# Performance work log

Hardware: AMD Instinct MI355X
Metric: run time of the kernel (lower is better)

The kernel has to match this reference:

```python
import jax, jax.numpy as jnp
import numpy as np

POOL = 7          # pooling_regions
NUM_ROIS = 4
FEAT = 2048
NUM_CLASSES = 21


def _adaptive_avg_pool(crop, out=POOL):
    # crop: [C, Hc, Wc] with concrete (Python int) spatial sizes.
    # torch adaptive_avg_pool2d bins: start=floor(i*S/out), end=ceil((i+1)*S/out)
    C, Hc, Wc = crop.shape
    cs = jnp.cumsum(jnp.cumsum(crop, axis=1), axis=2)
    cs = jnp.pad(cs, ((0, 0), (1, 0), (1, 0)))  # integral image [C, Hc+1, Wc+1]
    i = np.arange(out)
    hs = np.floor(i * Hc / out).astype(np.int32)
    he = np.ceil((i + 1) * Hc / out).astype(np.int32)
    ws = np.floor(i * Wc / out).astype(np.int32)
    we = np.ceil((i + 1) * Wc / out).astype(np.int32)
    S = (cs[:, he[:, None], we[None, :]] - cs[:, hs[:, None], we[None, :]]
         - cs[:, he[:, None], ws[None, :]] + cs[:, hs[:, None], ws[None, :]])
    area = ((he - hs)[:, None] * (we - ws)[None, :]).astype(crop.dtype)
    return S / area  # [C, out, out]


def setup_inputs() -> dict:
    key = jax.random.key(0)
    ks = jax.random.split(key, 8)
    H = W = 128
    base_x = jax.random.normal(ks[0], (1, FEAT, H, W), dtype=jnp.float32)
    # rows are (x, y, h, w); crop = base_x[:, :, x:x+w, y:y+h]; fixed in-bounds boxes
    rois = jnp.array([[0, 0, 96, 96], [10, 20, 64, 80], [30, 5, 50, 70], [64, 64, 64, 64]], dtype=jnp.int32)
    red = FEAT // 4  # 512
    flat = red * POOL * POOL  # 25088
    conv_w = jax.random.normal(ks[1], (red, FEAT), dtype=jnp.float32) * 0.02   # 1x1 conv kernel
    conv_b = jnp.zeros((red,), dtype=jnp.float32)
    d1_w = jax.random.normal(ks[2], (2 * FEAT, flat), dtype=jnp.float32) * 0.01
    d1_b = jnp.zeros((2 * FEAT,), dtype=jnp.float32)
    d2_w = jax.random.normal(ks[3], (FEAT, 2 * FEAT), dtype=jnp.float32) * 0.01
    d2_b = jnp.zeros((FEAT,), dtype=jnp.float32)
    d3_w = jax.random.normal(ks[4], (NUM_CLASSES, FEAT), dtype=jnp.float32) * 0.01
    d4_w = jax.random.normal(ks[5], (4 * (NUM_CLASSES - 1), FEAT), dtype=jnp.float32) * 0.01
    return {"base_x": base_x, "rois": rois, "conv_w": conv_w, "conv_b": conv_b,
            "d1_w": d1_w, "d1_b": d1_b, "d2_w": d2_w, "d2_b": d2_b,
            "d3_w": d3_w, "d4_w": d4_w}


def reference(base_x, rois, conv_w, conv_b, d1_w, d1_b, d2_w, d2_b, d3_w, d4_w):
    rois_np = np.asarray(rois)  # concrete ROI coordinates (data-dependent crop shapes)
    pooled = []
    for rid in range(rois_np.shape[0]):
        x, y, h, w = (int(v) for v in rois_np[rid])
        crop = base_x[0, :, x:x + w, y:y + h]           # [FEAT, w, h]
        pooled.append(_adaptive_avg_pool(crop))          # [FEAT, 7, 7]
    out_roi_pool = jnp.stack(pooled, axis=0)             # [4, FEAT, 7, 7]
    # 1x1 conv reduction FEAT -> FEAT//4
    red = jnp.einsum('rchw,oc->rohw', out_roi_pool, conv_w) + conv_b[None, :, None, None]
    flat = red.reshape(NUM_ROIS, -1)                     # [4, 512*7*7]
    h1 = jax.nn.relu(flat @ d1_w.T + d1_b)               # dropout = identity (eval)
    h2 = jax.nn.relu(h1 @ d2_w.T + d2_b)
    out_class = jax.nn.softmax(h2 @ d3_w.T, axis=1)      # [4, num_classes]
    out_regr = h2 @ d4_w.T                               # [4, 4*(num_classes-1)]
    return (out_class, out_regr)
```

## Files before the change

kernel.cpp:

```cpp
#include <hip/hip_runtime.h>
#include <math.h>

#define FEAT   2048
#define RED    512
#define NROI   4
#define FLATSZ 25088
#define H1SZ   4096
#define H2SZ   2048
#define NCLS   21
#define NREG   80

__device__ __forceinline__ float wave_reduce_sum(float v) {
#pragma unroll
    for (int off = 32; off >= 1; off >>= 1)
        v += __shfl_xor(v, off, 64);
    return v;
}

__global__ __launch_bounds__(64) void pool_kernel(const float* __restrict__ base_x,
                                                  const int* __restrict__ rois,
                                                  float* __restrict__ pooled) {
    int bx   = blockIdx.x;
    int hb   = bx % 7;
    int c    = (bx / 7) % FEAT;
    int r    = bx / (7 * FEAT);
    int lane = threadIdx.x;

    const int* roi = rois + r * 4;
    int x = roi[0], y = roi[1];
    int Wc = roi[2];
    int Hc = roi[3];

    int hs = (hb * Hc) / 7;
    int he = ((hb + 1) * Hc + 6) / 7;

    int j0 = lane, j1 = lane + 64;
    int b00 = -1, b01 = -1, b10 = -1, b11 = -1;
#pragma unroll
    for (int b = 0; b < 7; ++b) {
        int wsb = (b * Wc) / 7;
        int web = ((b + 1) * Wc + 6) / 7;
        if (j0 >= wsb && j0 < web) { if (b00 < 0) b00 = b; else b01 = b; }
        if (j1 >= wsb && j1 < web) { if (b10 < 0) b10 = b; else b11 = b; }
    }

    const float* plane = base_x + (size_t)c * 16384 + y;
    float s0 = 0.f, s1 = 0.f;
    for (int i = hs; i < he; ++i) {
        const float* rowp = plane + (size_t)(x + i) * 128;
        if (j0 < Wc) s0 += rowp[j0];
        if (j1 < Wc) s1 += rowp[j1];
    }

    float hspan = (float)(he - hs);
#pragma unroll
    for (int b = 0; b < 7; ++b) {
        float v = (((b == b00) || (b == b01)) ? s0 : 0.f) +
                  (((b == b10) || (b == b11)) ? s1 : 0.f);
        v = wave_reduce_sum(v);
        if (lane == 0) {
            int wsb = (b * Wc) / 7;
            int web = ((b + 1) * Wc + 6) / 7;
            float area = hspan * (float)(web - wsb);
            pooled[((size_t)r * FEAT + c) * 49 + hb * 7 + b] = v / area;
        }
    }
}

__global__ __launch_bounds__(256) void conv_kernel(const float* __restrict__ pooled,
                                                   const float* __restrict__ conv_w,
                                                   const float* __restrict__ conv_b,
                                                   float* __restrict__ flat) {
    int bx = blockIdx.x;
    int r  = bx >> 7;
    int o0 = (bx & 127) * 4;
    int tid  = threadIdx.x;
    int wave = tid >> 6, lane = tid & 63;
    int hw = lane < 49 ? lane : 48;

    const float* pp  = pooled + (size_t)r * FEAT * 49 + hw;
    const float* w0p = conv_w + (size_t)(o0 + 0) * FEAT;
    const float* w1p = conv_w + (size_t)(o0 + 1) * FEAT;
    const float* w2p = conv_w + (size_t)(o0 + 2) * FEAT;
    const float* w3p = conv_w + (size_t)(o0 + 3) * FEAT;

    float a0 = 0.f, a1 = 0.f, a2 = 0.f, a3 = 0.f;
    int c0 = wave * 512;
#pragma unroll 8
    for (int c = c0; c < c0 + 512; ++c) {
        float v = pp[(size_t)c * 49];
        a0 += w0p[c] * v;
        a1 += w1p[c] * v;
        a2 += w2p[c] * v;
        a3 += w3p[c] * v;
    }

    __shared__ float lds[4][4][64];
    lds[wave][0][lane] = a0;
    lds[wave][1][lane] = a1;
    lds[wave][2][lane] = a2;
    lds[wave][3][lane] = a3;
    __syncthreads();

    if (lane < 49) {
        int od = wave;
        float v = lds[0][od][lane] + lds[1][od][lane] + lds[2][od][lane] + lds[3][od][lane];
        flat[(size_t)r * FLATSZ + (size_t)(o0 + od) * 49 + lane] = v + conv_b[o0 + od];
    }
}

#define DOT4(a, b) ((a).x * (b).x + (a).y * (b).y + (a).z * (b).z + (a).w * (b).w)

template <int K4, int ACT_LD, int OUT_LD, bool RELU>
__global__ __launch_bounds__(256) void gemv_rows4(const float* __restrict__ act,
                                                  const float* __restrict__ w,
                                                  const float* __restrict__ bias,
                                                  float* __restrict__ out) {
    const int j0  = blockIdx.x * 4;
    const int tid = threadIdx.x;
    const int K   = K4 * 4;

    const float4* w0 = (const float4*)(w + (size_t)(j0 + 0) * K);
    const float4* w1 = (const float4*)(w + (size_t)(j0 + 1) * K);
    const float4* w2 = (const float4*)(w + (size_t)(j0 + 2) * K);
    const float4* w3 = (const float4*)(w + (size_t)(j0 + 3) * K);
    const float4* a0 = (const float4*)(act + 0 * (size_t)ACT_LD);
    const float4* a1 = (const float4*)(act + 1 * (size_t)ACT_LD);
    const float4* a2 = (const float4*)(act + 2 * (size_t)ACT_LD);
    const float4* a3 = (const float4*)(act + 3 * (size_t)ACT_LD);

    float acc[16];
#pragma unroll
    for (int i = 0; i < 16; ++i) acc[i] = 0.f;

    for (int k = tid; k < K4; k += 256) {
        float4 va0 = a0[k], va1 = a1[k], va2 = a2[k], va3 = a3[k];
        float4 vw0 = w0[k], vw1 = w1[k], vw2 = w2[k], vw3 = w3[k];
        acc[0]  += DOT4(vw0, va0); acc[1]  += DOT4(vw0, va1); acc[2]  += DOT4(vw0, va2); acc[3]  += DOT4(vw0, va3);
        acc[4]  += DOT4(vw1, va0); acc[5]  += DOT4(vw1, va1); acc[6]  += DOT4(vw1, va2); acc[7]  += DOT4(vw1, va3);
        acc[8]  += DOT4(vw2, va0); acc[9]  += DOT4(vw2, va1); acc[10] += DOT4(vw2, va2); acc[11] += DOT4(vw2, va3);
        acc[12] += DOT4(vw3, va0); acc[13] += DOT4(vw3, va1); acc[14] += DOT4(vw3, va2); acc[15] += DOT4(vw3, va3);
    }

#pragma unroll
    for (int i = 0; i < 16; ++i) acc[i] = wave_reduce_sum(acc[i]);

    __shared__ float lds[4][16];
    int wave = tid >> 6, lane = tid & 63;
    if (lane == 0) {
#pragma unroll
        for (int i = 0; i < 16; ++i) lds[wave][i] = acc[i];
    }
    __syncthreads();

    if (tid < 16) {
        float v  = lds[0][tid] + lds[1][tid] + lds[2][tid] + lds[3][tid];
        int   jj = tid >> 2, rr = tid & 3;
        int   j  = j0 + jj;
        v += bias[j];
        if (RELU) v = fmaxf(v, 0.f);
        out[(size_t)rr * OUT_LD + j] = v;
    }
}

__global__ __launch_bounds__(256) void head_kernel(const float* __restrict__ h2,
                                                   const float* __restrict__ d3_w,
                                                   const float* __restrict__ d4_w,
                                                   float* __restrict__ logits,
                                                   float* __restrict__ out) {
    int i = blockIdx.x;
    const float* wrow = (i < NCLS) ? (d3_w + (size_t)i * H2SZ)
                                   : (d4_w + (size_t)(i - NCLS) * H2SZ);
    int tid = threadIdx.x;
    const float4* w4 = (const float4*)wrow;
    const float4* a0 = (const float4*)(h2);
    const float4* a1 = (const float4*)(h2 + H2SZ);
    const float4* a2 = (const float4*)(h2 + 2 * H2SZ);
    const float4* a3 = (const float4*)(h2 + 3 * H2SZ);

    float acc0 = 0.f, acc1 = 0.f, acc2 = 0.f, acc3 = 0.f;
    for (int k = tid; k < 512; k += 256) {
        float4 w = w4[k];
        acc0 += DOT4(w, a0[k]);
        acc1 += DOT4(w, a1[k]);
        acc2 += DOT4(w, a2[k]);
        acc3 += DOT4(w, a3[k]);
    }
    acc0 = wave_reduce_sum(acc0);
    acc1 = wave_reduce_sum(acc1);
    acc2 = wave_reduce_sum(acc2);
    acc3 = wave_reduce_sum(acc3);

    __shared__ float lds[4][4];
    int wave = tid >> 6, lane = tid & 63;
    if (lane == 0) { lds[wave][0] = acc0; lds[wave][1] = acc1; lds[wave][2] = acc2; lds[wave][3] = acc3; }
    __syncthreads();

    if (tid < 4) {
        float v = lds[0][tid] + lds[1][tid] + lds[2][tid] + lds[3][tid];
        if (i < NCLS) logits[tid * NCLS + i] = v;
        else          out[NROI * NCLS + tid * NREG + (i - NCLS)] = v;
    }
}

__global__ __launch_bounds__(256) void softmax_kernel(const float* __restrict__ logits,
                                                      float* __restrict__ out) {
    int tid = threadIdx.x;
    int r = tid >> 6, lane = tid & 63;
    float v = (lane < NCLS) ? logits[r * NCLS + lane] : -INFINITY;
    float m = v;
#pragma unroll
    for (int off = 32; off >= 1; off >>= 1)
        m = fmaxf(m, __shfl_xor(m, off, 64));
    float e = (lane < NCLS) ? expf(v - m) : 0.f;
    float s = wave_reduce_sum(e);
    if (lane < NCLS) out[r * NCLS + lane] = e / s;
}

extern "C" void kernel_launch(void* const* d_in, const int* in_sizes, int n_in,
                              void* d_out, int out_size, void* d_ws, size_t ws_size,
                              hipStream_t stream) {
    (void)in_sizes; (void)n_in; (void)out_size; (void)ws_size;
    const float* base_x = (const float*)d_in[0];
    const int*   rois   = (const int*)d_in[1];
    const float* conv_w = (const float*)d_in[2];
    const float* conv_b = (const float*)d_in[3];
    const float* d1_w   = (const float*)d_in[4];
    const float* d1_b   = (const float*)d_in[5];
    const float* d2_w   = (const float*)d_in[6];
    const float* d2_b   = (const float*)d_in[7];
    const float* d3_w   = (const float*)d_in[8];
    const float* d4_w   = (const float*)d_in[9];
    float* out = (float*)d_out;

    char*  ws     = (char*)d_ws;
    float* pooled = (float*)(ws);
    float* flat   = (float*)(ws + 1605632);
    float* h1     = (float*)(ws + 2007040);
    float* h2     = (float*)(ws + 2072576);
    float* logits = (float*)(ws + 2105344);

    pool_kernel<<<NROI * FEAT * 7, 64, 0, stream>>>(base_x, rois, pooled);
    conv_kernel<<<NROI * (RED / 4), 256, 0, stream>>>(pooled, conv_w, conv_b, flat);
    gemv_rows4<FLATSZ / 4, FLATSZ, H1SZ, true><<<H1SZ / 4, 256, 0, stream>>>(flat, d1_w, d1_b, h1);
    gemv_rows4<H1SZ / 4, H1SZ, H2SZ, true><<<H2SZ / 4, 256, 0, stream>>>(h1, d2_w, d2_b, h2);
    head_kernel<<<NCLS + NREG, 256, 0, stream>>>(h2, d3_w, d4_w, logits, out);
    softmax_kernel<<<1, 256, 0, stream>>>(logits, out);
}
```

Measured before the change: 738.1 us.

## Restructure ROI pooling to one wave per channel with LDS column sums

The pooling kernel now assigns one wave per channel (four channels per 256-thread block) instead of one 64-thread block per channel and row-bin. Each wave computes per-column sums for all seven row bins, stores them in shared memory, and then 49 lanes reduce the column ranges, replacing the seven shuffle reductions per block. The aim is to cut block count and launch/reduction overhead and reuse loaded rows better. The GEMV and head loops also get unroll-by-2 hints and reordered loads, which may raise register pressure.

Result: faster. 701.1 us (-5.0%).

```diff
diff --git a/kernel.cpp b/kernel.cpp
--- a/kernel.cpp
+++ b/kernel.cpp
@@ -17,53 +17,60 @@
     return v;
 }
 
-__global__ __launch_bounds__(64) void pool_kernel(const float* __restrict__ base_x,
-                                                  const int* __restrict__ rois,
-                                                  float* __restrict__ pooled) {
+__global__ __launch_bounds__(256) void pool_kernel(const float* __restrict__ base_x,
+                                                   const int* __restrict__ rois,
+                                                   float* __restrict__ pooled) {
     int bx   = blockIdx.x;
-    int hb   = bx % 7;
-    int c    = (bx / 7) % FEAT;
-    int r    = bx / (7 * FEAT);
-    int lane = threadIdx.x;
+    int r    = bx >> 9;
+    int cg   = bx & 511;
+    int tid  = threadIdx.x;
+    int wave = tid >> 6, lane = tid & 63;
+    int c    = cg * 4 + wave;
 
     const int* roi = rois + r * 4;
     int x = roi[0], y = roi[1];
     int Wc = roi[2];
     int Hc = roi[3];
 
-    int hs = (hb * Hc) / 7;
-    int he = ((hb + 1) * Hc + 6) / 7;
-
+    __shared__ float cs[4][7][130];
+
+    const float* plane = base_x + (size_t)c * 16384 + y;
     int j0 = lane, j1 = lane + 64;
-    int b00 = -1, b01 = -1, b10 = -1, b11 = -1;
+    bool p0 = (j0 < Wc), p1 = (j1 < Wc);
+
 #pragma unroll
     for (int b = 0; b < 7; ++b) {
-        int wsb = (b * Wc) / 7;
-        int web = ((b + 1) * Wc + 6) / 7;
-        if (j0 >= wsb && j0 < web) { if (b00 < 0) b00 = b; else b01 = b; }
-        if (j1 >= wsb && j1 < web) { if (b10 < 0) b10 = b; else b11 = b; }
-    }
-
-    const float* plane = base_x + (size_t)c * 16384 + y;
-    float s0 = 0.f, s1 = 0.f;
-    for (int i = hs; i < he; ++i) {
-        const float* rowp = plane + (size_t)(x + i) * 128;
-        if (j0 < Wc) s0 += rowp[j0];
-        if (j1 < Wc) s1 += rowp[j1];
-    }
-
-    float hspan = (float)(he - hs);
-#pragma unroll
-    for (int b = 0; b < 7; ++b) {
-        float v = (((b == b00) || (b == b01)) ? s0 : 0.f) +
-                  (((b == b10) || (b == b11)) ? s1 : 0.f);
-        v = wave_reduce_sum(v);
-        if (lane == 0) {
-            int wsb = (b * Wc) / 7;
-            int web = ((b + 1) * Wc + 6) / 7;
-            float area = hspan * (float)(web - wsb);
-            pooled[((size_t)r * FEAT + c) * 49 + hb * 7 + b] = v / area;
+        int hs = (b * Hc) / 7;
+        int he = ((b + 1) * Hc + 6) / 7;
+        float s0 = 0.f, s1 = 0.f;
+        int i = hs;
+        for (; i + 2 <= he; i += 2) {
+            const float* r0 = plane + (size_t)(x + i) * 128;
+            float t0 = p0 ? r0[j0] : 0.f;
+            float t1 = p1 ? r0[j1] : 0.f;
+            float t2 = p0 ? r0[128 + j0] : 0.f;
+            float t3 = p1 ? r0[128 + j1] : 0.f;
+            s0 += t0 + t2;
+            s1 += t1 + t3;
         }
+        if (i < he) {
+            const float* r0 = plane + (size_t)(x + i) * 128;
+            if (p0) s0 += r0[j0];
+            if (p1) s1 += r0[j1];
+        }
+        cs[wave][b][j0] = s0;
+        cs[wave][b][j1] = s1;
+    }
+    __syncthreads();
+
+    if (lane < 49) {
+        int hb = lane / 7, wb = lane % 7;
+        int hs = (hb * Hc) / 7, he = ((hb + 1) * Hc + 6) / 7;
+        int ws = (wb * Wc) / 7, we = ((wb + 1) * Wc + 6) / 7;
+        float s = 0.f;
+        for (int k = ws; k < we; ++k) s += cs[wave][hb][k];
+        float area = (float)(he - hs) * (float)(we - ws);
+        pooled[((size_t)r * FEAT + c) * 49 + lane] = s / area;
     }
 }
 
@@ -133,9 +140,10 @@
 #pragma unroll
     for (int i = 0; i < 16; ++i) acc[i] = 0.f;
 
+#pragma unroll 2
     for (int k = tid; k < K4; k += 256) {
+        float4 vw0 = w0[k], vw1 = w1[k], vw2 = w2[k], vw3 = w3[k];
         float4 va0 = a0[k], va1 = a1[k], va2 = a2[k], va3 = a3[k];
-        float4 vw0 = w0[k], vw1 = w1[k], vw2 = w2[k], vw3 = w3[k];
         acc[0]  += DOT4(vw0, va0); acc[1]  += DOT4(vw0, va1); acc[2]  += DOT4(vw0, va2); acc[3]  += DOT4(vw0, va3);
         acc[4]  += DOT4(vw1, va0); acc[5]  += DOT4(vw1, va1); acc[6]  += DOT4(vw1, va2); acc[7]  += DOT4(vw1, va3);
         acc[8]  += DOT4(vw2, va0); acc[9]  += DOT4(vw2, va1); acc[10] += DOT4(vw2, va2); acc[11] += DOT4(vw2, va3);
@@ -179,6 +187,7 @@
     const float4* a3 = (const float4*)(h2 + 3 * H2SZ);
 
     float acc0 = 0.f, acc1 = 0.f, acc2 = 0.f, acc3 = 0.f;
+#pragma unroll 2
     for (int k = tid; k < 512; k += 256) {
         float4 w = w4[k];
         acc0 += DOT4(w, a0[k]);
@@ -240,7 +249,7 @@
     float* h2     = (float*)(ws + 2072576);
     float* logits = (float*)(ws + 2105344);
 
-    pool_kernel<<<NROI * FEAT * 7, 64, 0, stream>>>(base_x, rois, pooled);
+    pool_kernel<<<NROI * (FEAT / 4), 256, 0, stream>>>(base_x, rois, pooled);
     conv_kernel<<<NROI * (RED / 4), 256, 0, stream>>>(pooled, conv_w, conv_b, flat);
     gemv_rows4<FLATSZ / 4, FLATSZ, H1SZ, true><<<H1SZ / 4, 256, 0, stream>>>(flat, d1_w, d1_b, h1);
     gemv_rows4<H1SZ / 4, H1SZ, H2SZ, true><<<H2SZ / 4, 256, 0, stream>>>(h1, d2_w, d2_b, h2);
```
